# Optimization experiments

Hardware: AMD Instinct MI355X
Metric: run time of the kernel (lower is better)

Reference implementation:

```python
import jax, jax.numpy as jnp
import numpy as np
from jax import lax

B, CIN, COUT, H, W, K = 16, 256, 384, 56, 56, 3
HOUT = H - K + 1  # 54, valid conv
MAP_RADIUS = (COUT - 1) // 2  # 191
LFB_SIGMA = float(MAP_RADIUS)  # default lfb_sigma = map_radius.max()


def _lfb_kernel():
    # Gaussian lateral-feedback kernel over the 1D channel map (lfb_gauss)
    d = jnp.abs(jnp.arange(COUT, dtype=jnp.float32) - MAP_RADIUS)
    return jnp.exp(-(d ** 2) / (2.0 * LFB_SIGMA ** 2))


def setup_inputs() -> dict:
    key = jax.random.key(0)
    k1, k2 = jax.random.split(key)
    x = jax.random.normal(k1, (B, CIN, H, W), dtype=jnp.float32)
    stdv = 1.0 / np.sqrt(CIN * K * K)
    weight = jax.random.uniform(k2, (COUT, CIN, K, K), dtype=jnp.float32,
                                minval=-stdv, maxval=stdv)
    return {"x": x, "weight": weight}


def reference(x, weight):
    # out_sim = kernel_mult2d: plain valid conv2d, stride 1
    y = lax.conv_general_dilated(x, weight, window_strides=(1, 1), padding='VALID',
                                 dimension_numbers=('NCHW', 'OIHW', 'NCHW'))  # (B,COUT,54,54)
    # Competitive operates on (N, out_channels): flatten batch+spatial, channel-last
    yf = y.transpose(0, 2, 3, 1).reshape(-1, COUT)  # (N, C)
    # winner-take-all, k=1: binary mask of per-row max (non-differentiable, like torch compare)
    mx = jnp.max(yf, axis=1, keepdims=True)
    winner_mask = lax.stop_gradient((yf >= mx).astype(yf.dtype))
    # lateral feedback: pad channel map and conv1d with Gaussian kernel
    pad_pre = MAP_RADIUS
    pad_post = COUT - 1 - MAP_RADIUS
    lfb_in = jnp.pad(winner_mask, ((0, 0), (pad_pre, pad_post)))[:, None, :]  # (N,1,2C-1)
    kern = _lfb_kernel()[None, None, :]  # (1,1,C)
    lfb_out = lax.conv_general_dilated(lfb_in, kern, window_strides=(1,), padding='VALID',
                                       dimension_numbers=('NCH', 'OIH', 'NCH'))[:, 0, :]  # (N,C)
    lfb_out = jnp.clip(lfb_out, -1.0, 1.0)
    # lfb_y_gating: gate lateral-feedback output by activations
    out = lfb_out * yf
    return out.reshape(B, HOUT, HOUT, COUT).transpose(0, 3, 1, 2)
```

## Files before the change

### kernel.cpp

```cpp
#include <hip/hip_runtime.h>

#define CIN   256
#define COUT  384
#define HH    56
#define WW    56
#define HO    54
#define NB    16
#define NPIX  (NB*HO*HO)
#define KK    (CIN*9)
#define XCH   (HH*WW)
#define XIMG  (CIN*HH*WW)

#define BM 128
#define BN 128
#define NCHUNK (KK/32)
#define KGRP   (KK/8)
#define WPLANE (KGRP*COUT*8)

#define WS_Y_OFF (8u << 20)

typedef __bf16  bf16x8 __attribute__((ext_vector_type(8)));
typedef float   f32x4  __attribute__((ext_vector_type(4)));
typedef ushort  us8    __attribute__((ext_vector_type(8)));

__device__ __forceinline__ ushort rne_bf16(float f) {
    unsigned u = __float_as_uint(f);
    return (ushort)((u + 0x7FFFu + ((u >> 16) & 1u)) >> 16);
}
__device__ __forceinline__ void split3(float v, ushort& h1, ushort& h2, ushort& h3) {
    h1 = rne_bf16(v);
    float r1 = v - __uint_as_float((unsigned)h1 << 16);
    h2 = rne_bf16(r1);
    float r2 = r1 - __uint_as_float((unsigned)h2 << 16);
    h3 = rne_bf16(r2);
}

__global__ __launch_bounds__(256) void wsplit(const float* __restrict__ w,
                                              ushort* __restrict__ wg) {
    int idx = blockIdx.x * 256 + threadIdx.x;
    int cout = idx / KK, k = idx - cout * KK;
    ushort h1, h2, h3;
    split3(w[idx], h1, h2, h3);
    int base = ((k >> 3) * COUT + cout) * 8 + (k & 7);
    wg[base]              = h1;
    wg[WPLANE + base]     = h2;
    wg[2 * WPLANE + base] = h3;
}

__global__ __launch_bounds__(256, 2) void conv_mfma(const float* __restrict__ x,
                                                    const ushort* __restrict__ wg,
                                                    float* __restrict__ y) {
    __shared__ __align__(16) ushort As[3][4][128][8];
    __shared__ __align__(16) ushort Bs[3][4][128][8];
    __shared__ int offk[KK];

    const int tid = threadIdx.x;
    const int c0 = blockIdx.y * BM;
    const int p0 = blockIdx.x * BN;

    for (int k = tid; k < KK; k += 256) {
        int cin = k / 9, r = k - cin * 9;
        int dy = r / 3, dx = r - dy * 3;
        offk[k] = cin * XCH + dy * WW + dx;
    }

    const int nb  = tid & 127;
    const int gb0 = tid >> 7;
    int pbase;
    {
        int p = p0 + nb; if (p >= NPIX) p = NPIX - 1;
        int b = p / 2916, rem = p - b * 2916;
        int oy = rem / 54, ox = rem - oy * 54;
        pbase = b * XIMG + oy * WW + ox;
    }
    __syncthreads();

    const int lane = tid & 63;
    const int wv = tid >> 6;
    const int wr = wv >> 1, wc = wv & 1;
    const int l15 = lane & 15, lg = lane >> 4;
    const int mrow = wr * 64 + l15;
    const int ncol = wc * 64 + l15;

    f32x4 acc[4][4];
#pragma unroll
    for (int i = 0; i < 4; ++i)
#pragma unroll
        for (int j = 0; j < 4; ++j) acc[i][j] = (f32x4)0.f;

    float4 aPre[6];
    float  bPre[2][8];
    us8    bSpl[2][3];

    auto PREFETCH = [&](int c) {
#pragma unroll
        for (int r = 0; r < 6; ++r) {
            int flat = r * 256 + tid;
            int s = flat >> 9, rem = flat & 511;
            int g = rem >> 7, m = rem & 127;
            aPre[r] = *(const float4*)(wg + ((s * KGRP + (c * 4 + g)) * COUT + (c0 + m)) * 8);
        }
#pragma unroll
        for (int t = 0; t < 2; ++t) {
            int kb = c * 32 + (gb0 + 2 * t) * 8;
#pragma unroll
            for (int kk = 0; kk < 8; ++kk)
                bPre[t][kk] = x[pbase + offk[kb + kk]];
        }
    };

    auto SPLITB = [&]() {
#pragma unroll
        for (int t = 0; t < 2; ++t) {
            us8 h1v, h2v, h3v;
#pragma unroll
            for (int kk = 0; kk < 8; ++kk) {
                ushort a, b, c2;
                split3(bPre[t][kk], a, b, c2);
                h1v[kk] = a; h2v[kk] = b; h3v[kk] = c2;
            }
            bSpl[t][0] = h1v; bSpl[t][1] = h2v; bSpl[t][2] = h3v;
        }
    };

    auto WRITE = [&]() {
#pragma unroll
        for (int r = 0; r < 6; ++r) {
            int flat = r * 256 + tid;
            *(float4*)((ushort*)As + flat * 8) = aPre[r];
        }
#pragma unroll
        for (int t = 0; t < 2; ++t) {
            int g = gb0 + 2 * t;
#pragma unroll
            for (int s = 0; s < 3; ++s)
                *(us8*)&Bs[s][g][nb][0] = bSpl[t][s];
        }
    };

    auto COMPUTE = [&]() {
        bf16x8 af[3][4];
#pragma unroll
        for (int s = 0; s < 3; ++s)
#pragma unroll
            for (int mi = 0; mi < 4; ++mi)
                af[s][mi] = *(const bf16x8*)&As[s][lg][mrow + mi * 16][0];
#pragma unroll
        for (int sb = 0; sb < 3; ++sb) {
            bf16x8 bf[4];
#pragma unroll
            for (int ni = 0; ni < 4; ++ni)
                bf[ni] = *(const bf16x8*)&Bs[sb][lg][ncol + ni * 16][0];
#pragma unroll
            for (int sa = 0; sa + sb < 3; ++sa)
#pragma unroll
                for (int mi = 0; mi < 4; ++mi)
#pragma unroll
                    for (int ni = 0; ni < 4; ++ni)
                        acc[mi][ni] = __builtin_amdgcn_mfma_f32_16x16x32_bf16(
                            af[sa][mi], bf[ni], acc[mi][ni], 0, 0, 0);
        }
    };

    PREFETCH(0);
    SPLITB();
    WRITE();
    __syncthreads();

    for (int c = 0; ; ) {
        if (c + 1 < NCHUNK) { PREFETCH(c + 1); SPLITB(); }
        COMPUTE();
        if (++c == NCHUNK) break;
        __syncthreads();
        WRITE();
        __syncthreads();
    }

#pragma unroll
    for (int ni = 0; ni < 4; ++ni) {
        int col = p0 + wc * 64 + ni * 16 + l15;
        if (col < NPIX) {
#pragma unroll
            for (int mi = 0; mi < 4; ++mi) {
                int row0 = c0 + wr * 64 + mi * 16 + lg * 4;
#pragma unroll
                for (int j = 0; j < 4; ++j)
                    y[(row0 + j) * NPIX + col] = acc[mi][ni][j];
            }
        }
    }
}

__global__ __launch_bounds__(256) void gate(const float* __restrict__ y,
                                            float* __restrict__ out) {
    __shared__ float ys[COUT][33];
    __shared__ float gtab[COUT];
    __shared__ float pmax[8][32];
    __shared__ float mx[32];
    __shared__ int   wcnt[32];
    __shared__ int   wlist[32][4];

    const int tid = threadIdx.x;
    const int tx = tid & 31, ty = tid >> 5;
    const int p0 = blockIdx.x * 32;

    for (int k = tid; k < COUT; k += 256) {
        float d = (float)(k - 191);
        gtab[k] = expf(-d * d * (1.0f / (2.0f * 191.0f * 191.0f)));
    }
    if (ty == 0) wcnt[tx] = 0;

    for (int c = ty; c < COUT; c += 8)
        ys[c][tx] = y[c * NPIX + p0 + tx];
    __syncthreads();

    float m = -3.402823466e+38f;
    for (int c = ty; c < COUT; c += 8) m = fmaxf(m, ys[c][tx]);
    pmax[ty][tx] = m;
    __syncthreads();
    if (ty == 0) {
        float mm = pmax[0][tx];
#pragma unroll
        for (int r = 1; r < 8; ++r) mm = fmaxf(mm, pmax[r][tx]);
        mx[tx] = mm;
    }
    __syncthreads();

    const float mm = mx[tx];
    for (int c = ty; c < COUT; c += 8) {
        if (ys[c][tx] >= mm) {
            int pos = atomicAdd(&wcnt[tx], 1);
            if (pos < 4) wlist[tx][pos] = c;
        }
    }
    __syncthreads();

    const int p   = p0 + tx;
    const int b   = p / 2916;
    const int rem = p - b * 2916;
    const int obase = b * (COUT * 2916) + rem;
    const int L = min(wcnt[tx], 4);
    for (int c = ty; c < COUT; c += 8) {
        float lfb = 0.f;
        for (int i = 0; i < L; ++i) {
            int d = wlist[tx][i] - c + 191;
            if (d >= 0 && d < COUT) lfb += gtab[d];
        }
        lfb = fminf(lfb, 1.0f);
        out[obase + c * 2916] = lfb * ys[c][tx];
    }
}

extern "C" void kernel_launch(void* const* d_in, const int* in_sizes, int n_in,
                              void* d_out, int out_size, void* d_ws, size_t ws_size,
                              hipStream_t stream) {
    const float* x = (const float*)d_in[0];
    const float* w = (const float*)d_in[1];
    float* outp = (float*)d_out;

    ushort* wg = (ushort*)d_ws;
    float*  y  = (float*)((char*)d_ws + WS_Y_OFF);

    wsplit<<<(KK * COUT) / 256, 256, 0, stream>>>(w, wg);

    dim3 grid((NPIX + BN - 1) / BN, COUT / BM);
    conv_mfma<<<grid, 256, 0, stream>>>(x, wg, y);

    gate<<<NPIX / 32, 256, 0, stream>>>(y, outp);
}
```

Measured before the change: 939.1 us.

## Switch conv GEMM to 32x32x16 MFMA and move offset table to global

Replaces the 16x16x32 bf16 MFMA tiles with 32x32x16 MFMA (2x2 accumulators of 16 floats per wave), which changes the LDS fragment loads and the output store mapping. The im2col offset table moves from shared memory to a global buffer filled by a new small kernel and is read as int4 vectors. Launch bounds rise to 3 blocks per CU. Together these aim to cut LDS traffic per MFMA, shrink shared memory and raise occupancy, at the cost of an extra launch and global offset loads.

```diff
diff --git a/kernel.cpp b/kernel.cpp
--- a/kernel.cpp
+++ b/kernel.cpp
@@ -17,10 +17,11 @@
 #define KGRP   (KK/8)
 #define WPLANE (KGRP*COUT*8)
 
-#define WS_Y_OFF (8u << 20)
+#define WS_OFF_OFF (6u << 20)
+#define WS_Y_OFF   (8u << 20)
 
 typedef __bf16  bf16x8 __attribute__((ext_vector_type(8)));
-typedef float   f32x4  __attribute__((ext_vector_type(4)));
+typedef float   f32x16 __attribute__((ext_vector_type(16)));
 typedef ushort  us8    __attribute__((ext_vector_type(8)));
 
 __device__ __forceinline__ ushort rne_bf16(float f) {
@@ -47,22 +48,25 @@
     wg[2 * WPLANE + base] = h3;
 }
 
-__global__ __launch_bounds__(256, 2) void conv_mfma(const float* __restrict__ x,
+__global__ __launch_bounds__(256) void offk_init(int* __restrict__ offg) {
+    int k = blockIdx.x * 256 + threadIdx.x;
+    if (k < KK) {
+        int cin = k / 9, r = k - cin * 9;
+        int dy = r / 3, dx = r - dy * 3;
+        offg[k] = cin * XCH + dy * WW + dx;
+    }
+}
+
+__global__ __launch_bounds__(256, 3) void conv_mfma(const float* __restrict__ x,
                                                     const ushort* __restrict__ wg,
+                                                    const int* __restrict__ offg,
                                                     float* __restrict__ y) {
     __shared__ __align__(16) ushort As[3][4][128][8];
     __shared__ __align__(16) ushort Bs[3][4][128][8];
-    __shared__ int offk[KK];
 
     const int tid = threadIdx.x;
     const int c0 = blockIdx.y * BM;
     const int p0 = blockIdx.x * BN;
-
-    for (int k = tid; k < KK; k += 256) {
-        int cin = k / 9, r = k - cin * 9;
-        int dy = r / 3, dx = r - dy * 3;
-        offk[k] = cin * XCH + dy * WW + dx;
-    }
 
     const int nb  = tid & 127;
     const int gb0 = tid >> 7;
@@ -73,20 +77,19 @@
         int oy = rem / 54, ox = rem - oy * 54;
         pbase = b * XIMG + oy * WW + ox;
     }
-    __syncthreads();
 
     const int lane = tid & 63;
     const int wv = tid >> 6;
     const int wr = wv >> 1, wc = wv & 1;
-    const int l15 = lane & 15, lg = lane >> 4;
-    const int mrow = wr * 64 + l15;
-    const int ncol = wc * 64 + l15;
-
-    f32x4 acc[4][4];
-#pragma unroll
-    for (int i = 0; i < 4; ++i)
-#pragma unroll
-        for (int j = 0; j < 4; ++j) acc[i][j] = (f32x4)0.f;
+    const int l31 = lane & 31, lg = lane >> 5;
+    const int mrow = wr * 64 + l31;
+    const int ncol = wc * 64 + l31;
+
+    f32x16 acc[2][2];
+#pragma unroll
+    for (int i = 0; i < 2; ++i)
+#pragma unroll
+        for (int j = 0; j < 2; ++j) acc[i][j] = (f32x16)0.f;
 
     float4 aPre[6];
     float  bPre[2][8];
@@ -96,16 +99,24 @@
 #pragma unroll
         for (int r = 0; r < 6; ++r) {
             int flat = r * 256 + tid;
-            int s = flat >> 9, rem = flat & 511;
-            int g = rem >> 7, m = rem & 127;
+            int s = flat >> 9;
+            int g = (flat >> 7) & 3;
+            int m = flat & 127;
             aPre[r] = *(const float4*)(wg + ((s * KGRP + (c * 4 + g)) * COUT + (c0 + m)) * 8);
         }
 #pragma unroll
         for (int t = 0; t < 2; ++t) {
             int kb = c * 32 + (gb0 + 2 * t) * 8;
-#pragma unroll
-            for (int kk = 0; kk < 8; ++kk)
-                bPre[t][kk] = x[pbase + offk[kb + kk]];
+            int4 o0 = *(const int4*)(offg + kb);
+            int4 o1 = *(const int4*)(offg + kb + 4);
+            bPre[t][0] = x[pbase + o0.x];
+            bPre[t][1] = x[pbase + o0.y];
+            bPre[t][2] = x[pbase + o0.z];
+            bPre[t][3] = x[pbase + o0.w];
+            bPre[t][4] = x[pbase + o1.x];
+            bPre[t][5] = x[pbase + o1.y];
+            bPre[t][6] = x[pbase + o1.z];
+            bPre[t][7] = x[pbase + o1.w];
         }
     };
 
@@ -139,26 +150,32 @@
     };
 
     auto COMPUTE = [&]() {
-        bf16x8 af[3][4];
+        bf16x8 af[3][2][2];
 #pragma unroll
         for (int s = 0; s < 3; ++s)
 #pragma unroll
-            for (int mi = 0; mi < 4; ++mi)
-                af[s][mi] = *(const bf16x8*)&As[s][lg][mrow + mi * 16][0];
+            for (int mi = 0; mi < 2; ++mi)
+#pragma unroll
+                for (int ks = 0; ks < 2; ++ks)
+                    af[s][mi][ks] = *(const bf16x8*)&As[s][2 * ks + lg][mrow + mi * 32][0];
 #pragma unroll
         for (int sb = 0; sb < 3; ++sb) {
-            bf16x8 bf[4];
-#pragma unroll
-            for (int ni = 0; ni < 4; ++ni)
-                bf[ni] = *(const bf16x8*)&Bs[sb][lg][ncol + ni * 16][0];
+            bf16x8 bf[2][2];
+#pragma unroll
+            for (int ni = 0; ni < 2; ++ni)
+#pragma unroll
+                for (int ks = 0; ks < 2; ++ks)
+                    bf[ni][ks] = *(const bf16x8*)&Bs[sb][2 * ks + lg][ncol + ni * 32][0];
 #pragma unroll
             for (int sa = 0; sa + sb < 3; ++sa)
 #pragma unroll
-                for (int mi = 0; mi < 4; ++mi)
-#pragma unroll
-                    for (int ni = 0; ni < 4; ++ni)
-                        acc[mi][ni] = __builtin_amdgcn_mfma_f32_16x16x32_bf16(
-                            af[sa][mi], bf[ni], acc[mi][ni], 0, 0, 0);
+                for (int ks = 0; ks < 2; ++ks)
+#pragma unroll
+                    for (int mi = 0; mi < 2; ++mi)
+#pragma unroll
+                        for (int ni = 0; ni < 2; ++ni)
+                            acc[mi][ni] = __builtin_amdgcn_mfma_f32_32x32x16_bf16(
+                                af[sa][mi][ks], bf[ni][ks], acc[mi][ni], 0, 0, 0);
         }
     };
 
@@ -177,15 +194,17 @@
     }
 
 #pragma unroll
-    for (int ni = 0; ni < 4; ++ni) {
-        int col = p0 + wc * 64 + ni * 16 + l15;
+    for (int ni = 0; ni < 2; ++ni) {
+        int col = p0 + wc * 64 + ni * 32 + l31;
         if (col < NPIX) {
 #pragma unroll
-            for (int mi = 0; mi < 4; ++mi) {
-                int row0 = c0 + wr * 64 + mi * 16 + lg * 4;
-#pragma unroll
-                for (int j = 0; j < 4; ++j)
-                    y[(row0 + j) * NPIX + col] = acc[mi][ni][j];
+            for (int mi = 0; mi < 2; ++mi) {
+                int rb = c0 + wr * 64 + mi * 32 + 4 * lg;
+#pragma unroll
+                for (int reg = 0; reg < 16; ++reg) {
+                    int row = rb + (reg & 3) + 8 * (reg >> 2);
+                    y[row * NPIX + col] = acc[mi][ni][reg];
+                }
             }
         }
     }
@@ -258,13 +277,15 @@
     const float* w = (const float*)d_in[1];
     float* outp = (float*)d_out;
 
-    ushort* wg = (ushort*)d_ws;
-    float*  y  = (float*)((char*)d_ws + WS_Y_OFF);
+    ushort* wg   = (ushort*)d_ws;
+    int*    offg = (int*)((char*)d_ws + WS_OFF_OFF);
+    float*  y    = (float*)((char*)d_ws + WS_Y_OFF);
 
     wsplit<<<(KK * COUT) / 256, 256, 0, stream>>>(w, wg);
+    offk_init<<<(KK + 255) / 256, 256, 0, stream>>>(offg);
 
     dim3 grid((NPIX + BN - 1) / BN, COUT / BM);
-    conv_mfma<<<grid, 256, 0, stream>>>(x, wg, y);
+    conv_mfma<<<grid, 256, 0, stream>>>(x, wg, offg, y);
 
     gate<<<NPIX / 32, 256, 0, stream>>>(y, outp);
 }
```

Result: slower. 995.7 us (+6.0%).
